# Performance work log

Measured on AMD Instinct MI355X. Metric: run time of the kernel, lower is better.

## Reference

```python
import jax, jax.numpy as jnp
import numpy as np

N = 50000   # nodes
E = 800000  # edges
H = 128     # hidden_channels
L = 3       # num_layers - 2 GIN blocks
C = 1       # out_channels
G = 512     # graphs in batch
BN_EPS = 1e-5


def _bn(x, g, b, m, v):
    # BatchNorm1d in eval mode: running stats
    return g * (x - m) * jax.lax.rsqrt(v + BN_EPS) + b


def setup_inputs() -> dict:
    key = jax.random.key(0)
    ks = jax.random.split(key, 16)
    s = 0.05
    inp = {
        "x": jax.random.randint(ks[0], (N,), 0, 100),
        "edge_index": jax.random.randint(ks[1], (2, E), 0, N),
        "batch": jnp.sort(jax.random.randint(ks[2], (N,), 0, G)),
        "embed_table": jax.random.normal(ks[3], (100, H), jnp.float32) * s,
        # pre-conv BatchNorm1d (self.norms)
        "bn_g": jnp.ones((L, H), jnp.float32),
        "bn_b": jnp.zeros((L, H), jnp.float32),
        "bn_m": jax.random.normal(ks[4], (L, H), jnp.float32) * s,
        "bn_v": jax.random.uniform(ks[5], (L, H), jnp.float32, 0.5, 1.5),
        # self.lins
        "lin_w": jax.random.normal(ks[6], (L, H, H), jnp.float32) * s,
        "lin_b": jnp.zeros((L, H), jnp.float32),
        # GINConv eps (train_eps=True) and its MLP: Linear-BN-ReLU-Linear
        "eps": jnp.zeros((L,), jnp.float32),
        "mlp_w1": jax.random.normal(ks[7], (L, H, H), jnp.float32) * s,
        "mlp_b1": jnp.zeros((L, H), jnp.float32),
        "mbn_g": jnp.ones((L, H), jnp.float32),
        "mbn_b": jnp.zeros((L, H), jnp.float32),
        "mbn_m": jax.random.normal(ks[8], (L, H), jnp.float32) * s,
        "mbn_v": jax.random.uniform(ks[9], (L, H), jnp.float32, 0.5, 1.5),
        "mlp_w2": jax.random.normal(ks[10], (L, H, H), jnp.float32) * s,
        "mlp_b2": jnp.zeros((L, H), jnp.float32),
        # readout Linear
        "ro_w": jax.random.normal(ks[11], (H, C), jnp.float32) * s,
        "ro_b": jnp.zeros((C,), jnp.float32),
    }
    return inp


def reference(x, edge_index, batch, embed_table, bn_g, bn_b, bn_m, bn_v,
              lin_w, lin_b, eps, mlp_w1, mlp_b1, mbn_g, mbn_b, mbn_m, mbn_v,
              mlp_w2, mlp_b2, ro_w, ro_b):
    h = embed_table[x]                      # [N, H]
    src, dst = edge_index[0], edge_index[1]
    for i in range(L):
        h = _bn(h, bn_g[i], bn_b[i], bn_m[i], bn_v[i])
        h = jax.nn.relu(h @ lin_w[i] + lin_b[i])
        # dropout is identity in eval mode
        # GINConv: mlp((1+eps)*x + sum_{j in N(i)} x_j)
        agg = jax.ops.segment_sum(h[src], dst, num_segments=N)
        z = (1.0 + eps[i]) * h + agg
        z = jax.nn.relu(_bn(z @ mlp_w1[i] + mlp_b1[i], mbn_g[i], mbn_b[i], mbn_m[i], mbn_v[i]))
        h = z @ mlp_w2[i] + mlp_b2[i]
    out = h @ ro_w + ro_b                   # [N, C]
    return jax.ops.segment_sum(out, batch, num_segments=G)  # [G, C]
```

## Files before the change

kernel.cpp:

```cpp
#include <hip/hip_runtime.h>
#include <hip/hip_fp16.h>


#define HD 128
#define NLAYER 3
#define PITCH 136
#define EPB 2048

typedef _Float16 half8 __attribute__((ext_vector_type(8)));
typedef float    f32x4 __attribute__((ext_vector_type(4)));

__global__ void prep_weights(
    const float* __restrict__ bn_g, const float* __restrict__ bn_b,
    const float* __restrict__ bn_m, const float* __restrict__ bn_v,
    const float* __restrict__ lin_w, const float* __restrict__ lin_b,
    const float* __restrict__ mbn_g, const float* __restrict__ mbn_b,
    const float* __restrict__ mbn_m, const float* __restrict__ mbn_v,
    const float* __restrict__ mlp_w1, const float* __restrict__ mlp_b1,
    const float* __restrict__ mlp_w2,
    _Float16* __restrict__ wtl, float* __restrict__ fbl,
    _Float16* __restrict__ wt1, float* __restrict__ fb1,
    _Float16* __restrict__ wt2)
{
    const int l = blockIdx.x;
    const int t = threadIdx.x;
    __shared__ float sa[HD], sc[HD], sa2[HD];

    const int lb = l * HD;
    const int wb = l * HD * HD;
    float a  = bn_g[lb + t] * rsqrtf(bn_v[lb + t] + 1e-5f);
    float c  = bn_b[lb + t] - bn_m[lb + t] * a;
    float a2 = mbn_g[lb + t] * rsqrtf(mbn_v[lb + t] + 1e-5f);
    float c2 = mbn_b[lb + t] - mbn_m[lb + t] * a2;
    sa[t] = a; sc[t] = c; sa2[t] = a2;
    __syncthreads();

    float accb = lin_b[lb + t];
    for (int k = 0; k < HD; ++k) accb += sc[k] * lin_w[wb + k * HD + t];
    fbl[lb + t] = accb;
    fb1[lb + t] = a2 * mlp_b1[lb + t] + c2;

    for (int j = 0; j < HD; ++j) {
        wtl[wb + j * HD + t] = (_Float16)(sa[t] * lin_w[wb + t * HD + j]);
        wt1[wb + j * HD + t] = (_Float16)(sa2[j] * mlp_w1[wb + t * HD + j]);
        wt2[wb + j * HD + t] = (_Float16)(mlp_w2[wb + t * HD + j]);
    }
}

__global__ void count_deg(const int* __restrict__ dst, int* __restrict__ deg,
                          int e, int npr)
{
    int r = blockIdx.x & 7;
    int chunk = blockIdx.x >> 3;
    int lo = r * npr, hi = lo + npr;
    int base = chunk * EPB;
    int end = base + EPB; if (end > e) end = e;
    for (int i = base + threadIdx.x; i < end; i += 256) {
        int d = dst[i];
        if (d >= lo && d < hi) atomicAdd(&deg[d], 1);
    }
}

__global__ void fill_csr(const int* __restrict__ src, const int* __restrict__ dst,
                         int* __restrict__ cursor,
                         unsigned short* __restrict__ esrc, int e, int npr)
{
    int r = blockIdx.x & 7;
    int chunk = blockIdx.x >> 3;
    int lo = r * npr, hi = lo + npr;
    int base = chunk * EPB;
    int end = base + EPB; if (end > e) end = e;
    for (int i = base + threadIdx.x; i < end; i += 256) {
        int d = dst[i];
        int s = src[i];
        if (d >= lo && d < hi) {
            int p = atomicAdd(&cursor[d], 1);
            esrc[p] = (unsigned short)s;
        }
    }
}

__global__ void scan_blocks(const int* __restrict__ deg, int* __restrict__ excl,
                            int* __restrict__ partials, int n)
{
    __shared__ int wt[4];
    int t = threadIdx.x;
    int base = blockIdx.x * 1024 + t * 4;
    int v0 = (base + 0 < n) ? deg[base + 0] : 0;
    int v1 = (base + 1 < n) ? deg[base + 1] : 0;
    int v2 = (base + 2 < n) ? deg[base + 2] : 0;
    int v3 = (base + 3 < n) ? deg[base + 3] : 0;
    int s = v0 + v1 + v2 + v3;
    int lane = t & 63, w = t >> 6;
    int inc = s;
    #pragma unroll
    for (int d = 1; d < 64; d <<= 1) {
        int o = __shfl_up(inc, d);
        if (lane >= d) inc += o;
    }
    if (lane == 63) wt[w] = inc;
    __syncthreads();
    int off = 0;
    for (int i = 0; i < w; ++i) off += wt[i];
    int ex = off + inc - s;
    if (base + 0 < n) excl[base + 0] = ex; ex += v0;
    if (base + 1 < n) excl[base + 1] = ex; ex += v1;
    if (base + 2 < n) excl[base + 2] = ex; ex += v2;
    if (base + 3 < n) excl[base + 3] = ex;
    if (t == 255) partials[blockIdx.x] = off + inc;
}

__global__ void scan_add(int* __restrict__ rowst, int* __restrict__ cursor,
                         const int* __restrict__ partials, int nb, int n, int e)
{
    __shared__ int spfx[64];
    int t = threadIdx.x;
    if (t < 64) {
        int v = (t < nb) ? partials[t] : 0;
        int inc = v;
        #pragma unroll
        for (int d = 1; d < 64; d <<= 1) {
            int o = __shfl_up(inc, d);
            if (t >= d) inc += o;
        }
        spfx[t] = inc - v;
    }
    __syncthreads();
    int idx = blockIdx.x * blockDim.x + t;
    if (idx < n) {
        int v = rowst[idx] + spfx[idx >> 10];
        rowst[idx] = v;
        cursor[idx] = v;
    }
    if (idx == 0) rowst[n] = e;
}

__global__ __launch_bounds__(256, 3)
void lin_mfma(const float* __restrict__ Xf, const int* __restrict__ xidx,
              const _Float16* __restrict__ Wt, const float* __restrict__ B,
              _Float16* __restrict__ Y, int n)
{
    __shared__ __align__(16) _Float16 sA[64 * PITCH];
    const int t = threadIdx.x;
    const int lane = t & 63;
    const int w = t >> 6;
    const int rw_ = w >> 1, cw = w & 1;
    const int m = lane & 15, g = lane >> 4;
    const int tile = blockIdx.x * 64;

    {
        int row = t >> 2, q = t & 3;
        int gr = tile + row;
        _Float16* dst = &sA[row * PITCH + q * 32];
        if (gr < n) {
            int id = xidx[gr];
            const float4* src = reinterpret_cast<const float4*>(Xf + (size_t)id * HD) + q * 8;
            #pragma unroll
            for (int c = 0; c < 4; ++c) {
                float4 va = src[2 * c], vb = src[2 * c + 1];
                half8 h = {(_Float16)va.x, (_Float16)va.y, (_Float16)va.z, (_Float16)va.w,
                           (_Float16)vb.x, (_Float16)vb.y, (_Float16)vb.z, (_Float16)vb.w};
                *reinterpret_cast<half8*>(dst + c * 8) = h;
            }
        } else {
            half8 zz = {0, 0, 0, 0, 0, 0, 0, 0};
            #pragma unroll
            for (int c = 0; c < 4; ++c) *reinterpret_cast<half8*>(dst + c * 8) = zz;
        }
    }
    __syncthreads();

    half8 bf[4][4];
    #pragma unroll
    for (int ct4 = 0; ct4 < 4; ++ct4) {
        int ct = 4 * cw + ct4;
        #pragma unroll
        for (int kk = 0; kk < 4; ++kk)
            bf[ct4][kk] = *reinterpret_cast<const half8*>(
                Wt + (size_t)(16 * ct + m) * HD + kk * 32 + g * 8);
    }

    f32x4 acc[2][4];
    #pragma unroll
    for (int i = 0; i < 2; ++i)
        #pragma unroll
        for (int j = 0; j < 4; ++j) acc[i][j] = (f32x4){0.f, 0.f, 0.f, 0.f};

    #pragma unroll
    for (int rg2 = 0; rg2 < 2; ++rg2) {
        int rg = 2 * rw_ + rg2;
        #pragma unroll
        for (int kk = 0; kk < 4; ++kk) {
            half8 a = *reinterpret_cast<const half8*>(
                &sA[(16 * rg + m) * PITCH + kk * 32 + g * 8]);
            #pragma unroll
            for (int ct4 = 0; ct4 < 4; ++ct4)
                acc[rg2][ct4] = __builtin_amdgcn_mfma_f32_16x16x32_f16(
                    a, bf[ct4][kk], acc[rg2][ct4], 0, 0, 0);
        }
    }

    #pragma unroll
    for (int rg2 = 0; rg2 < 2; ++rg2) {
        int rg = 2 * rw_ + rg2;
        #pragma unroll
        for (int ct4 = 0; ct4 < 4; ++ct4) {
            int col = 16 * (4 * cw + ct4) + m;
            float bb = B[col];
            #pragma unroll
            for (int reg = 0; reg < 4; ++reg) {
                int r = tile + 16 * rg + 4 * g + reg;
                if (r < n) {
                    float v = fmaxf(acc[rg2][ct4][reg] + bb, 0.f);
                    Y[(size_t)r * HD + col] = (_Float16)v;
                }
            }
        }
    }
}

__global__ void aggregate_f16(const _Float16* __restrict__ h2,
                              const int* __restrict__ rowst,
                              const unsigned short* __restrict__ esrc,
                              const float* __restrict__ epsp,
                              int layer, _Float16* __restrict__ z, int n)
{
    int gw = (blockIdx.x * blockDim.x + threadIdx.x) >> 6;
    int lane = threadIdx.x & 63;
    if (gw >= n) return;
    float se = 1.0f + epsp[layer];
    int rs = __builtin_amdgcn_readfirstlane(rowst[gw]);
    int re = __builtin_amdgcn_readfirstlane(rowst[gw + 1]);
    const half2* hv = reinterpret_cast<const half2*>(h2);

    float2 own = __half22float2(hv[(size_t)gw * 64 + lane]);
    float ax[8], ay[8];
    ax[0] = se * own.x; ay[0] = se * own.y;
    #pragma unroll
    for (int k = 1; k < 8; ++k) { ax[k] = 0.f; ay[k] = 0.f; }

    for (int base = rs; base < re; base += 64) {
        int cnt = re - base; if (cnt > 64) cnt = 64;
        int eid = (base + lane < re) ? (int)esrc[base + lane] : 0;
        for (int j = 0; j < cnt; j += 16) {
            half2 t[16];
            #pragma unroll
            for (int k = 0; k < 16; ++k) {
                int idx = j + k; if (idx > cnt - 1) idx = cnt - 1;
                int sid = __builtin_amdgcn_readfirstlane(
                              __builtin_amdgcn_readlane(eid, idx));
                t[k] = hv[(size_t)sid * 64 + lane];
            }
            #pragma unroll
            for (int k = 0; k < 16; ++k) {
                if (j + k < cnt) {
                    float2 v = __half22float2(t[k]);
                    ax[k & 7] += v.x; ay[k & 7] += v.y;
                }
            }
        }
    }
    float ox = ((ax[0] + ax[1]) + (ax[2] + ax[3])) + ((ax[4] + ax[5]) + (ax[6] + ax[7]));
    float oy = ((ay[0] + ay[1]) + (ay[2] + ay[3])) + ((ay[4] + ay[5]) + (ay[6] + ay[7]));
    reinterpret_cast<half2*>(z)[(size_t)gw * 64 + lane] = __floats2half2_rn(ox, oy);
}

template<bool LAST>
__global__ __launch_bounds__(256, 3)
void mlp3(const _Float16* __restrict__ Z,
          const _Float16* __restrict__ Wt1, const float* __restrict__ B1,
          const _Float16* __restrict__ Wt2, const float* __restrict__ B2,
          const _Float16* __restrict__ Wt3, const float* __restrict__ B3,
          _Float16* __restrict__ Y,
          const float* __restrict__ rw, const float* __restrict__ rb,
          const int* __restrict__ batch, float* __restrict__ gout, int n)
{
    __shared__ __align__(16) _Float16 sA[64 * PITCH];
    __shared__ float sD[64][2];
    const int t = threadIdx.x;
    const int lane = t & 63;
    const int w = t >> 6;
    const int rw_ = w >> 1, cw = w & 1;
    const int m = lane & 15, g = lane >> 4;
    const int tile = blockIdx.x * 64;

    {
        int row = t >> 2, q = t & 3;
        int gr = tile + row;
        _Float16* dst = &sA[row * PITCH + q * 32];
        half8 zz = {0, 0, 0, 0, 0, 0, 0, 0};
        const half8* src = reinterpret_cast<const half8*>(Z + (size_t)gr * HD + q * 32);
        #pragma unroll
        for (int c = 0; c < 4; ++c)
            *reinterpret_cast<half8*>(dst + c * 8) = (gr < n) ? src[c] : zz;
    }
    __syncthreads();

    half8 bf[4][4];
    f32x4 acc[2][4];

    #pragma unroll
    for (int ct4 = 0; ct4 < 4; ++ct4) {
        int ct = 4 * cw + ct4;
        #pragma unroll
        for (int kk = 0; kk < 4; ++kk)
            bf[ct4][kk] = *reinterpret_cast<const half8*>(
                Wt1 + (size_t)(16 * ct + m) * HD + kk * 32 + g * 8);
    }
    #pragma unroll
    for (int i = 0; i < 2; ++i)
        #pragma unroll
        for (int j = 0; j < 4; ++j) acc[i][j] = (f32x4){0.f, 0.f, 0.f, 0.f};
    #pragma unroll
    for (int rg2 = 0; rg2 < 2; ++rg2) {
        int rg = 2 * rw_ + rg2;
        #pragma unroll
        for (int kk = 0; kk < 4; ++kk) {
            half8 a = *reinterpret_cast<const half8*>(
                &sA[(16 * rg + m) * PITCH + kk * 32 + g * 8]);
            #pragma unroll
            for (int ct4 = 0; ct4 < 4; ++ct4)
                acc[rg2][ct4] = __builtin_amdgcn_mfma_f32_16x16x32_f16(
                    a, bf[ct4][kk], acc[rg2][ct4], 0, 0, 0);
        }
    }
    __syncthreads();
    #pragma unroll
    for (int rg2 = 0; rg2 < 2; ++rg2) {
        int rg = 2 * rw_ + rg2;
        #pragma unroll
        for (int ct4 = 0; ct4 < 4; ++ct4) {
            int col = 16 * (4 * cw + ct4) + m;
            float bb = B1[col];
            #pragma unroll
            for (int reg = 0; reg < 4; ++reg) {
                int lr = 16 * rg + 4 * g + reg;
                sA[lr * PITCH + col] = (_Float16)fmaxf(acc[rg2][ct4][reg] + bb, 0.f);
            }
        }
    }
    __syncthreads();

    #pragma unroll
    for (int ct4 = 0; ct4 < 4; ++ct4) {
        int ct = 4 * cw + ct4;
        #pragma unroll
        for (int kk = 0; kk < 4; ++kk)
            bf[ct4][kk] = *reinterpret_cast<const half8*>(
                Wt2 + (size_t)(16 * ct + m) * HD + kk * 32 + g * 8);
    }
    f32x4 acc2[2][4];
    #pragma unroll
    for (int i = 0; i < 2; ++i)
        #pragma unroll
        for (int j = 0; j < 4; ++j) acc2[i][j] = (f32x4){0.f, 0.f, 0.f, 0.f};
    #pragma unroll
    for (int rg2 = 0; rg2 < 2; ++rg2) {
        int rg = 2 * rw_ + rg2;
        #pragma unroll
        for (int kk = 0; kk < 4; ++kk) {
            half8 a = *reinterpret_cast<const half8*>(
                &sA[(16 * rg + m) * PITCH + kk * 32 + g * 8]);
            #pragma unroll
            for (int ct4 = 0; ct4 < 4; ++ct4)
                acc2[rg2][ct4] = __builtin_amdgcn_mfma_f32_16x16x32_f16(
                    a, bf[ct4][kk], acc2[rg2][ct4], 0, 0, 0);
        }
    }

    if (LAST) {
        #pragma unroll
        for (int rg2 = 0; rg2 < 2; ++rg2) {
            int rg = 2 * rw_ + rg2;
            float pr[4] = {0.f, 0.f, 0.f, 0.f};
            #pragma unroll
            for (int ct4 = 0; ct4 < 4; ++ct4) {
                int col = 16 * (4 * cw + ct4) + m;
                float bb = B2[col], rr = rw[col];
                #pragma unroll
                for (int reg = 0; reg < 4; ++reg)
                    pr[reg] = fmaf(acc2[rg2][ct4][reg] + bb, rr, pr[reg]);
            }
            #pragma unroll
            for (int reg = 0; reg < 4; ++reg) {
                #pragma unroll
                for (int d = 1; d < 16; d <<= 1) pr[reg] += __shfl_xor(pr[reg], d);
            }
            if (m == 0) {
                #pragma unroll
                for (int reg = 0; reg < 4; ++reg)
                    sD[16 * rg + 4 * g + reg][cw] = pr[reg];
            }
        }
        __syncthreads();
        if (t < 64) {
            int row = tile + t;
            float v = sD[t][0] + sD[t][1] + rb[0];
            int b = (row < n) ? batch[row] : -1;
            if (row >= n) v = 0.f;
            #pragma unroll
            for (int d = 1; d < 64; d <<= 1) {
                int   ob = __shfl_up(b, d);
                float ov = __shfl_up(v, d);
                if (t >= d && ob == b) v += ov;
            }
            int nb2 = __shfl_down(b, 1);
            bool lastl = (t == 63) || (nb2 != b);
            if (lastl && b >= 0) atomicAdd(&gout[b], v);
        }
    } else {
        __syncthreads();
        #pragma unroll
        for (int rg2 = 0; rg2 < 2; ++rg2) {
            int rg = 2 * rw_ + rg2;
            #pragma unroll
            for (int ct4 = 0; ct4 < 4; ++ct4) {
                int col = 16 * (4 * cw + ct4) + m;
                float bb = B2[col];
                #pragma unroll
                for (int reg = 0; reg < 4; ++reg) {
                    int lr = 16 * rg + 4 * g + reg;
                    sA[lr * PITCH + col] = (_Float16)(acc2[rg2][ct4][reg] + bb);
                }
            }
        }
        __syncthreads();

        #pragma unroll
        for (int ct4 = 0; ct4 < 4; ++ct4) {
            int ct = 4 * cw + ct4;
            #pragma unroll
            for (int kk = 0; kk < 4; ++kk)
                bf[ct4][kk] = *reinterpret_cast<const half8*>(
                    Wt3 + (size_t)(16 * ct + m) * HD + kk * 32 + g * 8);
        }
        #pragma unroll
        for (int i = 0; i < 2; ++i)
            #pragma unroll
            for (int j = 0; j < 4; ++j) acc[i][j] = (f32x4){0.f, 0.f, 0.f, 0.f};
        #pragma unroll
        for (int rg2 = 0; rg2 < 2; ++rg2) {
            int rg = 2 * rw_ + rg2;
            #pragma unroll
            for (int kk = 0; kk < 4; ++kk) {
                half8 a = *reinterpret_cast<const half8*>(
                    &sA[(16 * rg + m) * PITCH + kk * 32 + g * 8]);
                #pragma unroll
                for (int ct4 = 0; ct4 < 4; ++ct4)
                    acc[rg2][ct4] = __builtin_amdgcn_mfma_f32_16x16x32_f16(
                        a, bf[ct4][kk], acc[rg2][ct4], 0, 0, 0);
            }
        }
        #pragma unroll
        for (int rg2 = 0; rg2 < 2; ++rg2) {
            int rg = 2 * rw_ + rg2;
            #pragma unroll
            for (int ct4 = 0; ct4 < 4; ++ct4) {
                int col = 16 * (4 * cw + ct4) + m;
                float bb = B3[col];
                #pragma unroll
                for (int reg = 0; reg < 4; ++reg) {
                    int r = tile + 16 * rg + 4 * g + reg;
                    if (r < n) {
                        float v = fmaxf(acc[rg2][ct4][reg] + bb, 0.f);
                        Y[(size_t)r * HD + col] = (_Float16)v;
                    }
                }
            }
        }
    }
}

extern "C" void kernel_launch(void* const* d_in, const int* in_sizes, int n_in,
                              void* d_out, int out_size, void* d_ws, size_t ws_size,
                              hipStream_t stream)
{
    const int N = in_sizes[0];
    const int E = in_sizes[1] / 2;
    const int G = out_size;

    const int*   x      = (const int*)d_in[0];
    const int*   ei     = (const int*)d_in[1];
    const int*   batch  = (const int*)d_in[2];
    const float* table  = (const float*)d_in[3];
    const float* bn_g   = (const float*)d_in[4];
    const float* bn_b   = (const float*)d_in[5];
    const float* bn_m   = (const float*)d_in[6];
    const float* bn_v   = (const float*)d_in[7];
    const float* lin_w  = (const float*)d_in[8];
    const float* lin_b  = (const float*)d_in[9];
    const float* epsv   = (const float*)d_in[10];
    const float* mlp_w1 = (const float*)d_in[11];
    const float* mlp_b1 = (const float*)d_in[12];
    const float* mbn_g  = (const float*)d_in[13];
    const float* mbn_b  = (const float*)d_in[14];
    const float* mbn_m  = (const float*)d_in[15];
    const float* mbn_v  = (const float*)d_in[16];
    const float* mlp_w2 = (const float*)d_in[17];
    const float* mlp_b2 = (const float*)d_in[18];
    const float* ro_w   = (const float*)d_in[19];
    const float* ro_b   = (const float*)d_in[20];

    const int* esrc_in = ei;
    const int* edst_in = ei + E;

    char* wsp = (char*)d_ws;
    size_t off = 0;
    auto alloc = [&](size_t bytes) {
        void* p = wsp + off;
        off += (bytes + 255) & ~(size_t)255;
        return p;
    };
    _Float16* bufA  = (_Float16*)alloc((size_t)N * HD * 2);
    _Float16* bufB  = (_Float16*)alloc((size_t)N * HD * 2);
    _Float16* wtl   = (_Float16*)alloc((size_t)NLAYER * HD * HD * 2);
    _Float16* wt1   = (_Float16*)alloc((size_t)NLAYER * HD * HD * 2);
    _Float16* wt2   = (_Float16*)alloc((size_t)NLAYER * HD * HD * 2);
    float*    fbl   = (float*)alloc((size_t)NLAYER * HD * 4);
    float*    fb1   = (float*)alloc((size_t)NLAYER * HD * 4);
    int*      deg   = (int*)alloc((size_t)N * 4);
    int*      rowst = (int*)alloc((size_t)(N + 1) * 4);
    int*      cursor= (int*)alloc((size_t)N * 4);
    unsigned short* esrc = (unsigned short*)alloc((size_t)E * 2);
    int*      part  = (int*)alloc(1024 * 4);
    (void)ws_size;

    hipMemsetAsync(deg, 0, (size_t)N * 4, stream);
    hipMemsetAsync(d_out, 0, (size_t)G * 4, stream);

    prep_weights<<<NLAYER, HD, 0, stream>>>(
        bn_g, bn_b, bn_m, bn_v, lin_w, lin_b,
        mbn_g, mbn_b, mbn_m, mbn_v, mlp_w1, mlp_b1, mlp_w2,
        wtl, fbl, wt1, fb1, wt2);

    const int npr = (N + 7) / 8;
    const int chunks = (E + EPB - 1) / EPB;
    count_deg<<<chunks * 8, 256, 0, stream>>>(edst_in, deg, E, npr);
    int nb = (N + 1023) / 1024;
    scan_blocks<<<nb, 256, 0, stream>>>(deg, rowst, part, N);
    scan_add<<<(N + 255) / 256, 256, 0, stream>>>(rowst, cursor, part, nb, N, E);
    fill_csr<<<chunks * 8, 256, 0, stream>>>(esrc_in, edst_in, cursor, esrc, E, npr);

    const int gemm_grid = (N + 63) / 64;
    const int wave_grid = (N + 3) / 4;

    lin_mfma<<<gemm_grid, 256, 0, stream>>>(table, x, wtl, fbl, bufB, N);

    for (int l = 0; l < NLAYER; ++l) {
        const _Float16* w1 = wt1 + (size_t)l * HD * HD;
        const float*    b1 = fb1 + (size_t)l * HD;
        const _Float16* w2 = wt2 + (size_t)l * HD * HD;
        const float*    b2 = mlp_b2 + (size_t)l * HD;

        aggregate_f16<<<wave_grid, 256, 0, stream>>>(
            bufB, rowst, esrc, epsv, l, bufA, N);

        if (l < NLAYER - 1) {
            const _Float16* w3 = wtl + (size_t)(l + 1) * HD * HD;
            const float*    b3 = fbl + (size_t)(l + 1) * HD;
            mlp3<false><<<gemm_grid, 256, 0, stream>>>(
                bufA, w1, b1, w2, b2, w3, b3, bufB,
                nullptr, nullptr, nullptr, nullptr, N);
        } else {
            mlp3<true><<<gemm_grid, 256, 0, stream>>>(
                bufA, w1, b1, w2, b2, nullptr, nullptr, nullptr,
                ro_w, ro_b, batch, (float*)d_out, N);
        }
    }
}
```

Measured before the change: 390.7 us.

## Fuse weight prep with degree count and widen MLP tiles to 128 rows

Merges the weight-preparation kernel and the degree-counting kernel into one launch, with the first blocks doing weight folding and the rest counting edges. The fused MLP kernel now runs 512 threads per block over 128-row tiles, doubling shared staging and fixing the readout segmented scan to work per wavefront. This saves one launch and amortizes weight fragment loads over more rows. In exchange it drops the 3-blocks-per-CU occupancy hint, and because the visible code maps warps to rows via w>>1, correctness depends on the hidden body indexing 8 warps properly.

```diff
diff --git a/kernel.cpp b/kernel.cpp
--- a/kernel.cpp
+++ b/kernel.cpp
@@ -10,7 +10,7 @@
 typedef _Float16 half8 __attribute__((ext_vector_type(8)));
 typedef float    f32x4 __attribute__((ext_vector_type(4)));
 
-__global__ void prep_weights(
+__global__ void prep_and_count(
     const float* __restrict__ bn_g, const float* __restrict__ bn_b,
     const float* __restrict__ bn_m, const float* __restrict__ bn_v,
     const float* __restrict__ lin_w, const float* __restrict__ lin_b,
@@ -20,44 +20,49 @@
     const float* __restrict__ mlp_w2,
     _Float16* __restrict__ wtl, float* __restrict__ fbl,
     _Float16* __restrict__ wt1, float* __restrict__ fb1,
-    _Float16* __restrict__ wt2)
-{
-    const int l = blockIdx.x;
+    _Float16* __restrict__ wt2,
+    const int* __restrict__ dst, int* __restrict__ deg, int e, int npr)
+{
+    __shared__ float sa[HD], sc[HD], sa2[HD];
     const int t = threadIdx.x;
-    __shared__ float sa[HD], sc[HD], sa2[HD];
-
-    const int lb = l * HD;
-    const int wb = l * HD * HD;
-    float a  = bn_g[lb + t] * rsqrtf(bn_v[lb + t] + 1e-5f);
-    float c  = bn_b[lb + t] - bn_m[lb + t] * a;
-    float a2 = mbn_g[lb + t] * rsqrtf(mbn_v[lb + t] + 1e-5f);
-    float c2 = mbn_b[lb + t] - mbn_m[lb + t] * a2;
-    sa[t] = a; sc[t] = c; sa2[t] = a2;
-    __syncthreads();
-
-    float accb = lin_b[lb + t];
-    for (int k = 0; k < HD; ++k) accb += sc[k] * lin_w[wb + k * HD + t];
-    fbl[lb + t] = accb;
-    fb1[lb + t] = a2 * mlp_b1[lb + t] + c2;
-
-    for (int j = 0; j < HD; ++j) {
-        wtl[wb + j * HD + t] = (_Float16)(sa[t] * lin_w[wb + t * HD + j]);
-        wt1[wb + j * HD + t] = (_Float16)(sa2[j] * mlp_w1[wb + t * HD + j]);
-        wt2[wb + j * HD + t] = (_Float16)(mlp_w2[wb + t * HD + j]);
-    }
-}
-
-__global__ void count_deg(const int* __restrict__ dst, int* __restrict__ deg,
-                          int e, int npr)
-{
-    int r = blockIdx.x & 7;
-    int chunk = blockIdx.x >> 3;
-    int lo = r * npr, hi = lo + npr;
-    int base = chunk * EPB;
-    int end = base + EPB; if (end > e) end = e;
-    for (int i = base + threadIdx.x; i < end; i += 256) {
-        int d = dst[i];
-        if (d >= lo && d < hi) atomicAdd(&deg[d], 1);
+
+    if (blockIdx.x < NLAYER) {
+        const int l = blockIdx.x;
+        const int lb = l * HD;
+        const int wb = l * HD * HD;
+        if (t < HD) {
+            float a  = bn_g[lb + t] * rsqrtf(bn_v[lb + t] + 1e-5f);
+            float c  = bn_b[lb + t] - bn_m[lb + t] * a;
+            float a2 = mbn_g[lb + t] * rsqrtf(mbn_v[lb + t] + 1e-5f);
+            sa[t] = a; sc[t] = c; sa2[t] = a2;
+        }
+        __syncthreads();
+        if (t < HD) {
+            float a2 = sa2[t];
+            float c2 = mbn_b[lb + t] - mbn_m[lb + t] * a2;
+
+            float accb = lin_b[lb + t];
+            for (int k = 0; k < HD; ++k) accb += sc[k] * lin_w[wb + k * HD + t];
+            fbl[lb + t] = accb;
+            fb1[lb + t] = a2 * mlp_b1[lb + t] + c2;
+
+            for (int j = 0; j < HD; ++j) {
+                wtl[wb + j * HD + t] = (_Float16)(sa[t] * lin_w[wb + t * HD + j]);
+                wt1[wb + j * HD + t] = (_Float16)(sa2[j] * mlp_w1[wb + t * HD + j]);
+                wt2[wb + j * HD + t] = (_Float16)(mlp_w2[wb + t * HD + j]);
+            }
+        }
+    } else {
+        int bid = blockIdx.x - NLAYER;
+        int r = bid & 7;
+        int chunk = bid >> 3;
+        int lo = r * npr, hi = lo + npr;
+        int base = chunk * EPB;
+        int end = base + EPB; if (end > e) end = e;
+        for (int i = base + t; i < end; i += 256) {
+            int d = dst[i];
+            if (d >= lo && d < hi) atomicAdd(&deg[d], 1);
+        }
     }
 }
 
@@ -266,7 +271,7 @@
 }
 
 template<bool LAST>
-__global__ __launch_bounds__(256, 3)
+__global__ __launch_bounds__(512)
 void mlp3(const _Float16* __restrict__ Z,
           const _Float16* __restrict__ Wt1, const float* __restrict__ B1,
           const _Float16* __restrict__ Wt2, const float* __restrict__ B2,
@@ -275,14 +280,14 @@
           const float* __restrict__ rw, const float* __restrict__ rb,
           const int* __restrict__ batch, float* __restrict__ gout, int n)
 {
-    __shared__ __align__(16) _Float16 sA[64 * PITCH];
-    __shared__ float sD[64][2];
+    __shared__ __align__(16) _Float16 sA[128 * PITCH];
+    __shared__ float sD[128][2];
     const int t = threadIdx.x;
     const int lane = t & 63;
     const int w = t >> 6;
     const int rw_ = w >> 1, cw = w & 1;
     const int m = lane & 15, g = lane >> 4;
-    const int tile = blockIdx.x * 64;
+    const int tile = blockIdx.x * 128;
 
     {
         int row = t >> 2, q = t & 3;
@@ -393,7 +398,7 @@
             }
         }
         __syncthreads();
-        if (t < 64) {
+        if (t < 128) {
             int row = tile + t;
             float v = sD[t][0] + sD[t][1] + rb[0];
             int b = (row < n) ? batch[row] : -1;
@@ -402,10 +407,10 @@
             for (int d = 1; d < 64; d <<= 1) {
                 int   ob = __shfl_up(b, d);
                 float ov = __shfl_up(v, d);
-                if (t >= d && ob == b) v += ov;
+                if (lane >= d && ob == b) v += ov;
             }
             int nb2 = __shfl_down(b, 1);
-            bool lastl = (t == 63) || (nb2 != b);
+            bool lastl = (lane == 63) || (nb2 != b);
             if (lastl && b >= 0) atomicAdd(&gout[b], v);
         }
     } else {
@@ -528,21 +533,22 @@
     hipMemsetAsync(deg, 0, (size_t)N * 4, stream);
     hipMemsetAsync(d_out, 0, (size_t)G * 4, stream);
 
-    prep_weights<<<NLAYER, HD, 0, stream>>>(
+    const int npr = (N + 7) / 8;
+    const int chunks = (E + EPB - 1) / EPB;
+    prep_and_count<<<NLAYER + chunks * 8, 256, 0, stream>>>(
         bn_g, bn_b, bn_m, bn_v, lin_w, lin_b,
         mbn_g, mbn_b, mbn_m, mbn_v, mlp_w1, mlp_b1, mlp_w2,
-        wtl, fbl, wt1, fb1, wt2);
-
-    const int npr = (N + 7) / 8;
-    const int chunks = (E + EPB - 1) / EPB;
-    count_deg<<<chunks * 8, 256, 0, stream>>>(edst_in, deg, E, npr);
+        wtl, fbl, wt1, fb1, wt2,
+        edst_in, deg, E, npr);
+
     int nb = (N + 1023) / 1024;
     scan_blocks<<<nb, 256, 0, stream>>>(deg, rowst, part, N);
     scan_add<<<(N + 255) / 256, 256, 0, stream>>>(rowst, cursor, part, nb, N, E);
     fill_csr<<<chunks * 8, 256, 0, stream>>>(esrc_in, edst_in, cursor, esrc, E, npr);
 
-    const int gemm_grid = (N + 63) / 64;
-    const int wave_grid = (N + 3) / 4;
+    const int gemm_grid   = (N + 63) / 64;
+    const int gemm_grid2  = (N + 127) / 128;
+    const int wave_grid   = (N + 3) / 4;
 
     lin_mfma<<<gemm_grid, 256, 0, stream>>>(table, x, wtl, fbl, bufB, N);
 
@@ -558,11 +564,11 @@
         if (l < NLAYER - 1) {
             const _Float16* w3 = wtl + (size_t)(l + 1) * HD * HD;
             const float*    b3 = fbl + (size_t)(l + 1) * HD;
-            mlp3<false><<<gemm_grid, 256, 0, stream>>>(
+            mlp3<false><<<gemm_grid2, 512, 0, stream>>>(
                 bufA, w1, b1, w2, b2, w3, b3, bufB,
                 nullptr, nullptr, nullptr, nullptr, N);
         } else {
-            mlp3<true><<<gemm_grid, 256, 0, stream>>>(
+            mlp3<true><<<gemm_grid2, 512, 0, stream>>>(
                 bufA, w1, b1, w2, b2, nullptr, nullptr, nullptr,
                 ro_w, ro_b, batch, (float*)d_out, N);
         }
```

Measured after the change: 380.1 us. -2.7%, faster.
